# Kernel tuning notes

Hardware: AMD Instinct MI355X
Metric: run time of the kernel (lower is better)

Reference implementation:

```python
import jax, jax.numpy as jnp
import numpy as np

D = 64          # data dimension
K = 16          # latent dimension
N = 65536       # number of samples
P = 2           # max_permutations
BETA = 10.0     # noise precision


def setup_inputs() -> dict:
    key = jax.random.key(0)
    kz, kw, ke, kp = jax.random.split(key, 4)
    W = jax.random.normal(kw, (D, K), jnp.float32)
    Z = jax.random.normal(kz, (N, K), jnp.float32)
    eps = (1.0 / BETA) * jax.random.normal(ke, (N, 1), jnp.float32)
    x = Z @ W.T + eps  # (N, D), matches the repo's generative model
    # one permutation of 0..D-1 per (dim a, permutation p)
    keys = jax.random.split(kp, D * P)
    perms = jax.vmap(lambda k: jax.random.permutation(k, D))(keys)
    perms = perms.reshape(D, P, D).astype(jnp.int32)
    return {"x": x, "W": W, "perms": perms}


def _masked_loss(x, W, perms):
    n = x.shape[0]
    log2pi = jnp.asarray(np.log(2.0 * np.pi), x.dtype)
    noise_eye = jnp.eye(D, dtype=x.dtype) / BETA
    total = jnp.zeros((), x.dtype)
    for a in range(D):
        m = a + 1
        loss_pred = jnp.zeros((n,), x.dtype)
        for p in range(P):
            perm = perms[a, p]
            Wp = W[perm]            # (D, K)
            xp = x[:, perm]         # (N, D)
            S = Wp @ Wp.T + noise_eye  # (D, D)
            if m == D:
                m_pred = jnp.zeros_like(xp)       # no conditioning set left
                v_pred = jnp.diagonal(S)          # (D,)
            else:
                S_mr = S[:m, m:]                              # (m, r)
                iS_rr = jnp.linalg.inv(S[m:, m:])             # (r, r)
                A = S_mr @ iS_rr                              # (m, r)
                m_pred = xp[:, m:] @ A.T                      # (N, m)
                v_pred = jnp.diagonal(S[:m, :m] - A @ S_mr.T) # (m,)
            diff = xp[:, :m] - m_pred
            log_p = -0.5 * jnp.log(v_pred) - 0.5 * log2pi - 0.5 * diff * diff / v_pred
            loss_pred = loss_pred + log_p.sum(axis=1)
        total = total + loss_pred.sum() / (P * m * n)
    return -total


def reference(x, W, perms):
    return _masked_loss(x, W, perms)
```

## Files before the change

### kernel.cpp

```cpp
#include <hip/hip_runtime.h>
#include <math.h>

#define D 64
#define K 16
#define PP 2
#define NN 65536
#define LOG2PI 1.8378770664093454
#define NOISE 0.1
#define NPAIR (D * PP)

#define RCHUNK 128
#define NCH (NN / RCHUNK)

__global__ __launch_bounds__(256) void gram_prep_kernel(const float* __restrict__ x,
                                                        const float* __restrict__ W,
                                                        const int* __restrict__ perms,
                                                        float* __restrict__ part,
                                                        int npart,
                                                        double* __restrict__ Ud,
                                                        double* __restrict__ dvd,
                                                        float* __restrict__ out) {
    const int tid = threadIdx.x;

    if (blockIdx.x < npart) {
        if (blockIdx.x == 0 && tid == 0) out[0] = 0.0f;
        __shared__ float xs[RCHUNK * D];
        const int ib = (tid >> 4) << 2;
        const int jb = (tid & 15) << 2;
        float acc[4][4];
#pragma unroll
        for (int u = 0; u < 4; ++u)
#pragma unroll
            for (int v = 0; v < 4; ++v) acc[u][v] = 0.0f;

        for (int cb = blockIdx.x; cb < NCH; cb += npart) {
            const float4* src = (const float4*)(x + (size_t)cb * RCHUNK * D);
            float4* dst = (float4*)xs;
#pragma unroll
            for (int u = 0; u < 8; ++u)
                dst[tid + 256 * u] = src[tid + 256 * u];
            __syncthreads();
#pragma unroll 4
            for (int r = 0; r < RCHUNK; ++r) {
                const float4 xi = *(const float4*)&xs[r * D + ib];
                const float4 xj = *(const float4*)&xs[r * D + jb];
                float a0[4] = {xi.x, xi.y, xi.z, xi.w};
                float b0[4] = {xj.x, xj.y, xj.z, xj.w};
#pragma unroll
                for (int u = 0; u < 4; ++u)
#pragma unroll
                    for (int v = 0; v < 4; ++v)
                        acc[u][v] = fmaf(a0[u], b0[v], acc[u][v]);
            }
            __syncthreads();
        }
        float* p = part + (size_t)blockIdx.x * (D * D);
#pragma unroll
        for (int u = 0; u < 4; ++u)
#pragma unroll
            for (int v = 0; v < 4; ++v)
                p[(ib + u) * D + (jb + v)] = acc[u][v];
        return;
    }

    const int pair = blockIdx.x - npart;
    const int m = pair / PP + 1;
    const int wave = tid >> 6;
    const int lane = tid & 63;

    __shared__ int perm[D];
    __shared__ float Wp[D][K + 1];
    __shared__ float Wz[D][K + 1];
    __shared__ double Mlds[K][K + 1];
    __shared__ double Minv[K][K + 1];
    __shared__ double dvp[4][D];

    if (tid < D) perm[tid] = perms[pair * D + tid];
    __syncthreads();
    for (int e = tid; e < D * K; e += 256) {
        int i = e >> 4, k = e & (K - 1);
        float w = W[perm[i] * K + k];
        Wp[i][k] = w;
        Wz[i][k] = (i >= m) ? w : 0.0f;
    }
    __syncthreads();

    {
        const int k1 = tid >> 4, k2 = tid & 15;
        double s = (k1 == k2) ? NOISE : 0.0;
#pragma unroll
        for (int sr = 0; sr < D; ++sr)
            s += (double)Wz[sr][k1] * (double)Wz[sr][k2];
        Mlds[k1][k2] = s;
    }
    __syncthreads();

    if (wave == 0) {
        const int r = lane & 15;
        const int ch = lane >> 4;
        double a[8];
#pragma unroll
        for (int j = 0; j < 8; ++j) {
            if (ch < 2) a[j] = Mlds[r][ch * 8 + j];
            else a[j] = ((ch - 2) * 8 + j == r) ? 1.0 : 0.0;
        }
        for (int k = 0; k < K; ++k) {
            const int chk = k >> 3;
            const int rk = k & 7;
            double colk = a[rk];
            double fme = __shfl(colk, (chk << 4) | r, 64);
            double piv = __shfl(colk, (chk << 4) | k, 64);
            double pinv = 1.0 / piv;
            double p[8];
#pragma unroll
            for (int j = 0; j < 8; ++j)
                p[j] = __shfl(a[j], (ch << 4) | k, 64) * pinv;
            if (r == k) {
#pragma unroll
                for (int j = 0; j < 8; ++j) a[j] = p[j];
            } else {
#pragma unroll
                for (int j = 0; j < 8; ++j) a[j] -= fme * p[j];
            }
        }
        if (ch >= 2)
#pragma unroll
            for (int j = 0; j < 8; ++j) Minv[r][(ch - 2) * 8 + j] = a[j];
    }
    __syncthreads();

    {
        const int j = tid & 63;
        const int kb = tid >> 6;
        double* Up = Ud + (size_t)pair * (K * D);
        double pdv = 0.0;
#pragma unroll
        for (int u = 0; u < 4; ++u) {
            const int k = kb + 4 * u;
            double s = 0.0;
#pragma unroll
            for (int k2 = 0; k2 < K; ++k2)
                s += Minv[k][k2] * (double)Wp[j][k2];
            Up[k * D + j] = s;
            pdv += (double)Wp[j][k] * s;
        }
        dvp[kb][j] = pdv;
    }
    __syncthreads();
    if (tid < D)
        dvd[(size_t)pair * D + tid] = dvp[0][tid] + dvp[1][tid] + dvp[2][tid] + dvp[3][tid];
}

__global__ __launch_bounds__(256) void reduce_kernel(const float* __restrict__ part,
                                                     int npart,
                                                     float* __restrict__ Gf) {
    const int tid = threadIdx.x;
    const int le = tid >> 4;
    const int sub = tid & 15;
    const int e = blockIdx.x * 16 + le;
    __shared__ double ps[16][17];
    double s0 = 0.0, s1 = 0.0;
    for (int b = sub; b < npart; b += 32)
        s0 += (double)part[(size_t)b * (D * D) + e];
    for (int b = sub + 16; b < npart; b += 32)
        s1 += (double)part[(size_t)b * (D * D) + e];
    ps[le][sub] = s0 + s1;
    __syncthreads();
    if (sub == 0) {
        double t = 0.0;
#pragma unroll
        for (int i = 0; i < 16; ++i) t += ps[le][i];
        Gf[e] = (float)t;
    }
}

__global__ __launch_bounds__(256) void pair2_kernel(const float* __restrict__ W,
                                                    const int* __restrict__ perms,
                                                    const float* __restrict__ Gf,
                                                    const double* __restrict__ Ud,
                                                    const double* __restrict__ dvd,
                                                    float* __restrict__ out) {
    const int pair = blockIdx.x;
    const int m = pair / PP + 1;
    const int tid = threadIdx.x;

    __shared__ int perm[D];
    __shared__ float Wz[D][K + 1];
    __shared__ float Gp[D][D + 1];
    __shared__ double Y[K][D + 1];
    __shared__ double Z[K][K + 1];
    __shared__ double Ush[K][D + 1];
    __shared__ double qp[4][D];

    if (tid < D) perm[tid] = perms[pair * D + tid];
    __syncthreads();
    for (int e = tid; e < D * K; e += 256) {
        int i = e >> 4, k = e & (K - 1);
        float w = W[perm[i] * K + k];
        Wz[i][k] = (i >= m) ? w : 0.0f;
    }
    for (int e = tid; e < D * D; e += 256) {
        int i = e >> 6, t = e & 63;
        Gp[i][t] = Gf[perm[i] * D + perm[t]];
    }
    for (int e = tid; e < K * D; e += 256)
        Ush[e >> 6][e & 63] = Ud[(size_t)pair * (K * D) + e];
    __syncthreads();

    {
        const int j = tid & 63;
        const int kb = tid >> 6;
        double s0 = 0.0, s1 = 0.0, s2 = 0.0, s3 = 0.0;
#pragma unroll
        for (int sr = 0; sr < D; ++sr) {
            const double g = (double)Gp[sr][j];
            s0 += (double)Wz[sr][kb] * g;
            s1 += (double)Wz[sr][kb + 4] * g;
            s2 += (double)Wz[sr][kb + 8] * g;
            s3 += (double)Wz[sr][kb + 12] * g;
        }
        Y[kb][j] = s0;
        Y[kb + 4][j] = s1;
        Y[kb + 8][j] = s2;
        Y[kb + 12][j] = s3;
    }
    __syncthreads();

    {
        const int k1 = tid >> 4, k2 = tid & 15;
        double s = 0.0;
#pragma unroll
        for (int sr = 0; sr < D; ++sr)
            s += Y[k1][sr] * (double)Wz[sr][k2];
        Z[k1][k2] = s;
    }
    __syncthreads();

    {
        const int lane4 = tid & 3;
        const int j = tid >> 2;
        double t1 = 0.0, t2 = 0.0;
#pragma unroll
        for (int k1 = lane4; k1 < K; k1 += 4) {
            const double uj = Ush[k1][j];
            t1 += uj * Y[k1][j];
            double zs = 0.0;
#pragma unroll
            for (int k2 = 0; k2 < K; ++k2) zs += Z[k1][k2] * Ush[k2][j];
            t2 += uj * zs;
        }
        qp[lane4][j] = -2.0 * t1 + t2;
    }
    __syncthreads();

    if (tid < D) {
        const int j = tid;
        double tj = 0.0;
        if (j < m) {
            const double dv = dvd[(size_t)pair * D + j];
            const double v = NOISE * (1.0 + dv);
            const double q =
                (double)Gp[j][j] + qp[0][j] + qp[1][j] + qp[2][j] + qp[3][j];
            tj = -0.5 * log(v) - 0.5 * LOG2PI - 0.5 * q / (v * (double)NN);
        }
#pragma unroll
        for (int off = 32; off > 0; off >>= 1) tj += __shfl_down(tj, off, 64);
        if (tid == 0) atomicAdd(out, (float)(-tj / (double)(PP * m)));
    }
}

extern "C" void kernel_launch(void* const* d_in, const int* in_sizes, int n_in,
                              void* d_out, int out_size, void* d_ws, size_t ws_size,
                              hipStream_t stream) {
    const float* x = (const float*)d_in[0];
    const float* W = (const float*)d_in[1];
    const int* perms = (const int*)d_in[2];

    char* ws = (char*)d_ws;
    float* Gf = (float*)ws;
    double* Ud = (double*)(ws + 16384);
    double* dvd = (double*)(ws + 16384 + NPAIR * K * D * sizeof(double));
    const size_t fixedsz =
        16384 + (size_t)NPAIR * K * D * sizeof(double) + (size_t)NPAIR * D * sizeof(double);
    float* part = (float*)(ws + fixedsz);

    int npart = NCH;
    {
        size_t avail = (ws_size > fixedsz) ? (ws_size - fixedsz) : 0;
        int fit = (int)(avail / (D * D * sizeof(float)));
        if (fit < npart) npart = fit;
        if (npart < 1) npart = 1;
    }

    gram_prep_kernel<<<npart + NPAIR, 256, 0, stream>>>(x, W, perms, part, npart,
                                                        Ud, dvd, (float*)d_out);
    reduce_kernel<<<256, 256, 0, stream>>>(part, npart, Gf);
    pair2_kernel<<<NPAIR, 256, 0, stream>>>(W, perms, Gf, Ud, dvd, (float*)d_out);
}
```

Measured before the change: 100.3 us.

## Use 8x8 per-thread Gram tiles with wave-split rows and LDS reduction

The Gram accumulation now has each wave cover the full 64x64 output, with each lane holding an 8x8 tile instead of a 4x4 tile, so register reuse per LDS load doubles. Each wave handles a quarter of the rows in a chunk, and the four per-wave partial sums are combined through shared memory before the partial is written out. The pair kernel also reads Wz as float4 (the padding is dropped so the rows stay aligned) and prefetches dvd early. The costs are 64 accumulator registers per thread, which may lower occupancy, and an extra shared-memory reduction step per block.

```diff
diff --git a/kernel.cpp b/kernel.cpp
--- a/kernel.cpp
+++ b/kernel.cpp
@@ -21,17 +21,19 @@
                                                         double* __restrict__ dvd,
                                                         float* __restrict__ out) {
     const int tid = threadIdx.x;
+    const int wave = tid >> 6;
+    const int lane = tid & 63;
 
     if (blockIdx.x < npart) {
         if (blockIdx.x == 0 && tid == 0) out[0] = 0.0f;
         __shared__ float xs[RCHUNK * D];
-        const int ib = (tid >> 4) << 2;
-        const int jb = (tid & 15) << 2;
-        float acc[4][4];
-#pragma unroll
-        for (int u = 0; u < 4; ++u)
-#pragma unroll
-            for (int v = 0; v < 4; ++v) acc[u][v] = 0.0f;
+        const int i0 = (lane >> 3) << 3;
+        const int j0 = (lane & 7) << 3;
+        float acc[8][8];
+#pragma unroll
+        for (int u = 0; u < 8; ++u)
+#pragma unroll
+            for (int v = 0; v < 8; ++v) acc[u][v] = 0.0f;
 
         for (int cb = blockIdx.x; cb < NCH; cb += npart) {
             const float4* src = (const float4*)(x + (size_t)cb * RCHUNK * D);
@@ -40,37 +42,61 @@
             for (int u = 0; u < 8; ++u)
                 dst[tid + 256 * u] = src[tid + 256 * u];
             __syncthreads();
-#pragma unroll 4
-            for (int r = 0; r < RCHUNK; ++r) {
-                const float4 xi = *(const float4*)&xs[r * D + ib];
-                const float4 xj = *(const float4*)&xs[r * D + jb];
-                float a0[4] = {xi.x, xi.y, xi.z, xi.w};
-                float b0[4] = {xj.x, xj.y, xj.z, xj.w};
-#pragma unroll
-                for (int u = 0; u < 4; ++u)
-#pragma unroll
-                    for (int v = 0; v < 4; ++v)
-                        acc[u][v] = fmaf(a0[u], b0[v], acc[u][v]);
+            const float4* xr = (const float4*)xs;
+#pragma unroll 2
+            for (int rr = 0; rr < 32; ++rr) {
+                const int r = (wave << 5) + rr;
+                const float4 a0 = xr[(r << 4) + (i0 >> 2)];
+                const float4 a1 = xr[(r << 4) + (i0 >> 2) + 1];
+                const float4 b0 = xr[(r << 4) + (j0 >> 2)];
+                const float4 b1 = xr[(r << 4) + (j0 >> 2) + 1];
+                const float av[8] = {a0.x, a0.y, a0.z, a0.w, a1.x, a1.y, a1.z, a1.w};
+                const float bv[8] = {b0.x, b0.y, b0.z, b0.w, b1.x, b1.y, b1.z, b1.w};
+#pragma unroll
+                for (int u = 0; u < 8; ++u)
+#pragma unroll
+                    for (int v = 0; v < 8; ++v)
+                        acc[u][v] = fmaf(av[u], bv[v], acc[u][v]);
             }
             __syncthreads();
         }
+        float* red = xs;
+        if (wave < 2) {
+            float* base = red + (wave << 12);
+#pragma unroll
+            for (int u = 0; u < 8; ++u) {
+                float4 w0 = {acc[u][0], acc[u][1], acc[u][2], acc[u][3]};
+                float4 w1 = {acc[u][4], acc[u][5], acc[u][6], acc[u][7]};
+                *(float4*)&base[(i0 + u) * D + j0] = w0;
+                *(float4*)&base[(i0 + u) * D + j0 + 4] = w1;
+            }
+        }
+        __syncthreads();
+        if (wave >= 2) {
+            float* base = red + ((wave - 2) << 12);
+#pragma unroll
+            for (int u = 0; u < 8; ++u) {
+                float4 w0 = *(const float4*)&base[(i0 + u) * D + j0];
+                float4 w1 = *(const float4*)&base[(i0 + u) * D + j0 + 4];
+                w0.x += acc[u][0]; w0.y += acc[u][1]; w0.z += acc[u][2]; w0.w += acc[u][3];
+                w1.x += acc[u][4]; w1.y += acc[u][5]; w1.z += acc[u][6]; w1.w += acc[u][7];
+                *(float4*)&base[(i0 + u) * D + j0] = w0;
+                *(float4*)&base[(i0 + u) * D + j0 + 4] = w1;
+            }
+        }
+        __syncthreads();
         float* p = part + (size_t)blockIdx.x * (D * D);
-#pragma unroll
-        for (int u = 0; u < 4; ++u)
-#pragma unroll
-            for (int v = 0; v < 4; ++v)
-                p[(ib + u) * D + (jb + v)] = acc[u][v];
+        for (int e = tid; e < D * D; e += 256)
+            p[e] = red[e] + red[4096 + e];
         return;
     }
 
     const int pair = blockIdx.x - npart;
     const int m = pair / PP + 1;
-    const int wave = tid >> 6;
-    const int lane = tid & 63;
 
     __shared__ int perm[D];
     __shared__ float Wp[D][K + 1];
-    __shared__ float Wz[D][K + 1];
+    __shared__ float Wz[D][K];
     __shared__ double Mlds[K][K + 1];
     __shared__ double Minv[K][K + 1];
     __shared__ double dvp[4][D];
@@ -185,13 +211,16 @@
     const int tid = threadIdx.x;
 
     __shared__ int perm[D];
-    __shared__ float Wz[D][K + 1];
+    __shared__ float Wz[D][K];
     __shared__ float Gp[D][D + 1];
     __shared__ double Y[K][D + 1];
     __shared__ double Z[K][K + 1];
     __shared__ double Ush[K][D + 1];
     __shared__ double qp[4][D];
 
+    double dvv = 0.0;
+    if (tid < D) dvv = dvd[(size_t)pair * D + tid];
+
     if (tid < D) perm[tid] = perms[pair * D + tid];
     __syncthreads();
     for (int e = tid; e < D * K; e += 256) {
@@ -213,16 +242,17 @@
         double s0 = 0.0, s1 = 0.0, s2 = 0.0, s3 = 0.0;
 #pragma unroll
         for (int sr = 0; sr < D; ++sr) {
+            const float4 wv = *(const float4*)&Wz[sr][4 * kb];
             const double g = (double)Gp[sr][j];
-            s0 += (double)Wz[sr][kb] * g;
-            s1 += (double)Wz[sr][kb + 4] * g;
-            s2 += (double)Wz[sr][kb + 8] * g;
-            s3 += (double)Wz[sr][kb + 12] * g;
-        }
-        Y[kb][j] = s0;
-        Y[kb + 4][j] = s1;
-        Y[kb + 8][j] = s2;
-        Y[kb + 12][j] = s3;
+            s0 += (double)wv.x * g;
+            s1 += (double)wv.y * g;
+            s2 += (double)wv.z * g;
+            s3 += (double)wv.w * g;
+        }
+        Y[4 * kb][j] = s0;
+        Y[4 * kb + 1][j] = s1;
+        Y[4 * kb + 2][j] = s2;
+        Y[4 * kb + 3][j] = s3;
     }
     __syncthreads();
 
@@ -257,8 +287,7 @@
         const int j = tid;
         double tj = 0.0;
         if (j < m) {
-            const double dv = dvd[(size_t)pair * D + j];
-            const double v = NOISE * (1.0 + dv);
+            const double v = NOISE * (1.0 + dvv);
             const double q =
                 (double)Gp[j][j] + qp[0][j] + qp[1][j] + qp[2][j] + qp[3][j];
             tj = -0.5 * log(v) - 0.5 * LOG2PI - 0.5 * q / (v * (double)NN);
```

Result: no change. 99.53 us (-0.8%).
